# Performance work log

Measured on AMD Instinct MI355X. Metric: run time of the kernel, lower is better.

The kernel has to match this reference:

```python
import jax, jax.numpy as jnp
import numpy as np

B, S, C = 4, 2048, 1024
E, H = 1024, 16
D = E // H  # head_dim = 64


def setup_inputs() -> dict:
    key = jax.random.key(0)
    k1, k2, k3, k4, k5 = jax.random.split(key, 5)
    s = 1.0 / np.sqrt(C)
    return {
        "x": jax.random.normal(k1, (B, S, C), dtype=jnp.float32),
        "w_qkv": jax.random.uniform(k2, (C, 3 * E), minval=-s, maxval=s, dtype=jnp.float32),
        "b_qkv": jax.random.uniform(k3, (3 * E,), minval=-s, maxval=s, dtype=jnp.float32),
        "w_out": jax.random.uniform(k4, (E, E), minval=-1.0 / np.sqrt(E), maxval=1.0 / np.sqrt(E), dtype=jnp.float32),
        "b_out": jax.random.uniform(k5, (E,), minval=-1.0 / np.sqrt(E), maxval=1.0 / np.sqrt(E), dtype=jnp.float32),
    }


def reference(x, w_qkv, b_qkv, w_out, b_out):
    b, s, _ = x.shape
    qkv = x @ w_qkv + b_qkv                      # [B,S,3E]
    qkv = qkv.reshape(b, s, 3, H, D)
    q = qkv[:, :, 0].transpose(0, 2, 1, 3)       # [B,H,S,D]
    k = qkv[:, :, 1].transpose(0, 2, 1, 3)
    v = qkv[:, :, 2].transpose(0, 2, 1, 3)
    scale = jnp.asarray(D, x.dtype) ** 0.5
    scores = jnp.einsum("bhqd,bhkd->bhqk", q, k) / scale
    attn = jax.nn.softmax(scores, axis=-1)       # dropout is identity in eval mode
    out = jnp.einsum("bhqk,bhkd->bhqd", attn, v)
    out = out.transpose(0, 2, 1, 3).reshape(b, s, E)
    return out @ w_out + b_out
```

## Files before the change

kernel.cpp:

```cpp
#include <hip/hip_runtime.h>


typedef _Float16 f16;
typedef f16 f16x2 __attribute__((ext_vector_type(2)));
typedef f16 f16x4 __attribute__((ext_vector_type(4)));
typedef f16 f16x8 __attribute__((ext_vector_type(8)));
typedef float f32x4 __attribute__((ext_vector_type(4)));

typedef const __attribute__((address_space(1))) void* gas_ptr;
typedef __attribute__((address_space(3))) void* lds_ptr;

__device__ __forceinline__ void load_lds16(const void* g, void* s) {
  __builtin_amdgcn_global_load_lds((gas_ptr)g, (lds_ptr)s, 16, 0, 0);
}

__device__ __forceinline__ f32x4 mfma16(f16x8 a, f16x8 b, f32x4 c) {
  return __builtin_amdgcn_mfma_f32_16x16x32_f16(a, b, c, 0, 0, 0);
}

__device__ __forceinline__ f32x4 mfma16k16(f16x4 a, f16x4 b, f32x4 c) {
  return __builtin_amdgcn_mfma_f32_16x16x16f16(a, b, c, 0, 0, 0);
}

__device__ __forceinline__ f16x2 pk2(float a, float b) {
  return __builtin_bit_cast(f16x2, __builtin_amdgcn_cvt_pkrtz(a, b));
}

__global__ __launch_bounds__(256) void cvt_x(const float* __restrict__ in, f16* __restrict__ out) {
  int i = blockIdx.x * 256 + threadIdx.x;
  const float4* p = (const float4*)in;
  float4 a = p[2 * i], b = p[2 * i + 1];
  f16x8 o;
  o[0] = (f16)a.x; o[1] = (f16)a.y; o[2] = (f16)a.z; o[3] = (f16)a.w;
  o[4] = (f16)b.x; o[5] = (f16)b.y; o[6] = (f16)b.z; o[7] = (f16)b.w;
  *(f16x8*)(out + 8 * (long)i) = o;
}

__global__ __launch_bounds__(256) void tconv(const float* __restrict__ in, f16* __restrict__ out,
                                             int R, int C) {
  __shared__ float t[32][33];
  int c0 = blockIdx.x * 32, r0 = blockIdx.y * 32;
  int tx = threadIdx.x, ty = threadIdx.y;
#pragma unroll
  for (int j = 0; j < 4; ++j)
    t[ty + 8 * j][tx] = in[(long)(r0 + ty + 8 * j) * C + c0 + tx];
  __syncthreads();
#pragma unroll
  for (int j = 0; j < 4; ++j)
    out[(long)(c0 + ty + 8 * j) * R + r0 + tx] = (f16)t[tx][ty + 8 * j];
}

__global__ __launch_bounds__(256) void qkv_gemm(const f16* __restrict__ A, const f16* __restrict__ BT,
                                                const float* __restrict__ bias,
                                                f16* __restrict__ Qs, f16* __restrict__ Kk,
                                                f16* __restrict__ Vt) {
  __shared__ __align__(16) f16 lA[128 * 32];
  __shared__ __align__(16) f16 lB[128 * 32];
  const int K = 1024;
  int tid = threadIdx.x, w = tid >> 6, lane = tid & 63, l16 = lane & 15, quad = lane >> 4;
  int wm = (w >> 1) * 64, wn = (w & 1) * 64;
  int blockM = blockIdx.x * 128, blockN = blockIdx.y * 128;
  f32x4 acc[4][4] = {};

  for (int k0 = 0; k0 < K; k0 += 32) {
    __syncthreads();
#pragma unroll
    for (int i = 0; i < 2; ++i) {
      int c = (i * 4 + w) * 64 + lane;
      load_lds16(A + (blockM + (c >> 2)) * K + k0 + (c & 3) * 8, lA + (i * 4 + w) * 512);
      load_lds16(BT + (blockN + (c >> 2)) * K + k0 + (c & 3) * 8, lB + (i * 4 + w) * 512);
    }
    __syncthreads();
    f16x8 af[4], bf[4];
#pragma unroll
    for (int mb = 0; mb < 4; ++mb) af[mb] = *(const f16x8*)&lA[(wm + mb * 16 + l16) * 32 + quad * 8];
#pragma unroll
    for (int nb = 0; nb < 4; ++nb) bf[nb] = *(const f16x8*)&lB[(wn + nb * 16 + l16) * 32 + quad * 8];
#pragma unroll
    for (int mb = 0; mb < 4; ++mb)
#pragma unroll
      for (int nb = 0; nb < 4; ++nb)
        acc[mb][nb] = mfma16(af[mb], bf[nb], acc[mb][nb]);
  }

  int which = blockIdx.y >> 3;
  const float SCALE = 0.18033688011112042f;
#pragma unroll
  for (int nb = 0; nb < 4; ++nb) {
    int col = blockN + wn + nb * 16 + l16;
    int hd = col & 1023, h = hd >> 6, d = hd & 63;
    float bv = bias[col];
#pragma unroll
    for (int mb = 0; mb < 4; ++mb) {
      int row0 = blockM + wm + mb * 16 + quad * 4;
      int b = row0 >> 11, s0 = row0 & 2047;
      if (which == 2) {
        f16x2 a = pk2(acc[mb][nb][0] + bv, acc[mb][nb][1] + bv);
        f16x2 c = pk2(acc[mb][nb][2] + bv, acc[mb][nb][3] + bv);
        *(f16x4*)&Vt[((b * 16 + h) * 64 + d) * 2048 + s0] =
            __builtin_shufflevector(a, c, 0, 1, 2, 3);
      } else if (which == 0) {
#pragma unroll
        for (int r = 0; r < 4; ++r)
          Qs[((b * 16 + h) * 2048 + s0 + r) * 64 + d] = (f16)((acc[mb][nb][r] + bv) * SCALE);
      } else {
#pragma unroll
        for (int r = 0; r < 4; ++r)
          Kk[((b * 16 + h) * 2048 + s0 + r) * 64 + d] = (f16)(acc[mb][nb][r] + bv);
      }
    }
  }
}

__global__ __launch_bounds__(256) void attn(const f16* __restrict__ Qs, const f16* __restrict__ Kk,
                                            const f16* __restrict__ Vt, f16* __restrict__ ctx) {
  __shared__ __align__(16) f16 lK[2][64 * 72];
  __shared__ __align__(16) f16 lV[2][64 * 72];
  int qt = blockIdx.x, bh = blockIdx.y;
  int tid = threadIdx.x, lane = tid & 63, l16 = lane & 15, quad = lane >> 4;
  int w = tid >> 6;
  const f16* Qbase = Qs + ((long)bh * 2048 + qt * 256 + w * 64) * 64;
  const f16* Kbh = Kk + (long)bh * 2048 * 64;
  const f16* Vbh = Vt + (long)bh * 64 * 2048;

  f16x8 qf[4][2];
#pragma unroll
  for (int rb = 0; rb < 4; ++rb)
#pragma unroll
    for (int ks = 0; ks < 2; ++ks)
      qf[rb][ks] = *(const f16x8*)(Qbase + (rb * 16 + l16) * 64 + ks * 32 + quad * 8);

  f32x4 of[4][4] = {};
  f32x4 osum[4] = {};
  const f16 one = (f16)1.f;
  const f16x4 vone = {one, one, one, one};

  int c0 = tid, c1 = 256 + tid;
  int r0s = c0 >> 3, o0 = (c0 & 7) * 8;
  int r1s = c1 >> 3, o1 = (c1 & 7) * 8;

  *(float4*)&lK[0][r0s * 72 + o0] = *(const float4*)(Kbh + r0s * 64 + o0);
  *(float4*)&lK[0][r1s * 72 + o1] = *(const float4*)(Kbh + r1s * 64 + o1);
  *(float4*)&lV[0][r0s * 72 + o0] = *(const float4*)(Vbh + (long)r0s * 2048 + o0);
  *(float4*)&lV[0][r1s * 72 + o1] = *(const float4*)(Vbh + (long)r1s * 2048 + o1);
  __syncthreads();

  for (int kt = 0; kt < 32; ++kt) {
    int cur = kt & 1, nxt = cur ^ 1;

    float4 pk0, pk1, pv0, pv1;
    if (kt < 31) {
      int kb0 = (kt + 1) * 64;
      pk0 = *(const float4*)(Kbh + (kb0 + r0s) * 64 + o0);
      pk1 = *(const float4*)(Kbh + (kb0 + r1s) * 64 + o1);
      pv0 = *(const float4*)(Vbh + (long)r0s * 2048 + kb0 + o0);
      pv1 = *(const float4*)(Vbh + (long)r1s * 2048 + kb0 + o1);
    }

#pragma unroll
    for (int kb = 0; kb < 4; ++kb) {
      f16x8 kf0 = *(const f16x8*)&lK[cur][(kb * 16 + l16) * 72 + quad * 8];
      f16x8 kf1 = *(const f16x8*)&lK[cur][(kb * 16 + l16) * 72 + 32 + quad * 8];

      f16x4 pa[4];
#pragma unroll
      for (int rb = 0; rb < 4; ++rb) {
        f32x4 z = {};
        z = mfma16(kf0, qf[rb][0], z);
        z = mfma16(kf1, qf[rb][1], z);
        float p0 = __builtin_amdgcn_exp2f(z[0]);
        float p1 = __builtin_amdgcn_exp2f(z[1]);
        float p2 = __builtin_amdgcn_exp2f(z[2]);
        float p3 = __builtin_amdgcn_exp2f(z[3]);
        pa[rb] = __builtin_shufflevector(pk2(p0, p1), pk2(p2, p3), 0, 1, 2, 3);
      }

#pragma unroll
      for (int db = 0; db < 4; ++db) {
        f16x4 vf = *(const f16x4*)&lV[cur][(db * 16 + l16) * 72 + kb * 16 + quad * 4];
#pragma unroll
        for (int rb = 0; rb < 4; ++rb)
          of[rb][db] = mfma16k16(pa[rb], vf, of[rb][db]);
      }
#pragma unroll
      for (int rb = 0; rb < 4; ++rb)
        osum[rb] = mfma16k16(pa[rb], vone, osum[rb]);
    }

    if (kt < 31) {
      *(float4*)&lK[nxt][r0s * 72 + o0] = pk0;
      *(float4*)&lK[nxt][r1s * 72 + o1] = pk1;
      *(float4*)&lV[nxt][r0s * 72 + o0] = pv0;
      *(float4*)&lV[nxt][r1s * 72 + o1] = pv1;
      __syncthreads();
    }
  }

  int b = bh >> 4, h = bh & 15;
  long token0 = (long)b * 2048 + qt * 256 + w * 64;
#pragma unroll
  for (int rb = 0; rb < 4; ++rb) {
    float inv[4];
#pragma unroll
    for (int r = 0; r < 4; ++r) inv[r] = 1.0f / osum[rb][r];
#pragma unroll
    for (int db = 0; db < 4; ++db)
#pragma unroll
      for (int r = 0; r < 4; ++r)
        ctx[(token0 + rb * 16 + quad * 4 + r) * 1024 + h * 64 + db * 16 + l16] =
            (f16)(of[rb][db][r] * inv[r]);
  }
}

__global__ __launch_bounds__(256) void proj_gemm(const f16* __restrict__ A, const f16* __restrict__ BT,
                                                 const float* __restrict__ bias,
                                                 float* __restrict__ out) {
  __shared__ __align__(16) f16 lA[128 * 32];
  __shared__ __align__(16) f16 lB[128 * 32];
  const int K = 1024;
  int tid = threadIdx.x, w = tid >> 6, lane = tid & 63, l16 = lane & 15, quad = lane >> 4;
  int wm = (w >> 1) * 64, wn = (w & 1) * 64;
  int blockM = blockIdx.x * 128, blockN = blockIdx.y * 128;
  f32x4 acc[4][4] = {};

  for (int k0 = 0; k0 < K; k0 += 32) {
    __syncthreads();
#pragma unroll
    for (int i = 0; i < 2; ++i) {
      int c = (i * 4 + w) * 64 + lane;
      load_lds16(A + (blockM + (c >> 2)) * K + k0 + (c & 3) * 8, lA + (i * 4 + w) * 512);
      load_lds16(BT + (blockN + (c >> 2)) * K + k0 + (c & 3) * 8, lB + (i * 4 + w) * 512);
    }
    __syncthreads();
    f16x8 af[4], bf[4];
#pragma unroll
    for (int mb = 0; mb < 4; ++mb) af[mb] = *(const f16x8*)&lA[(wm + mb * 16 + l16) * 32 + quad * 8];
#pragma unroll
    for (int nb = 0; nb < 4; ++nb) bf[nb] = *(const f16x8*)&lB[(wn + nb * 16 + l16) * 32 + quad * 8];
#pragma unroll
    for (int mb = 0; mb < 4; ++mb)
#pragma unroll
      for (int nb = 0; nb < 4; ++nb)
        acc[mb][nb] = mfma16(af[mb], bf[nb], acc[mb][nb]);
  }

#pragma unroll
  for (int nb = 0; nb < 4; ++nb) {
    int col = blockN + wn + nb * 16 + l16;
    float bv = bias[col];
#pragma unroll
    for (int mb = 0; mb < 4; ++mb) {
#pragma unroll
      for (int r = 0; r < 4; ++r) {
        int row = blockM + wm + mb * 16 + quad * 4 + r;
        out[(long)row * 1024 + col] = acc[mb][nb][r] + bv;
      }
    }
  }
}

extern "C" void kernel_launch(void* const* d_in, const int* in_sizes, int n_in,
                              void* d_out, int out_size, void* d_ws, size_t ws_size,
                              hipStream_t stream) {
  const float* x     = (const float*)d_in[0];
  const float* w_qkv = (const float*)d_in[1];
  const float* b_qkv = (const float*)d_in[2];
  const float* w_out = (const float*)d_in[3];
  const float* b_out = (const float*)d_in[4];
  float* out = (float*)d_out;

  char* ws = (char*)d_ws;
  f16* xh    = (f16*)(ws);
  f16* ctx   = (f16*)(ws);
  f16* wqkvT = (f16*)(ws + 16777216);
  f16* woutT = (f16*)(ws + 23068672);
  f16* Qs    = (f16*)(ws + 25165824);
  f16* Kk    = (f16*)(ws + 41943040);
  f16* Vt    = (f16*)(ws + 58720256);

  cvt_x<<<4096, 256, 0, stream>>>(x, xh);
  tconv<<<dim3(96, 32), dim3(32, 8), 0, stream>>>(w_qkv, wqkvT, 1024, 3072);
  tconv<<<dim3(32, 32), dim3(32, 8), 0, stream>>>(w_out, woutT, 1024, 1024);
  qkv_gemm<<<dim3(64, 24), 256, 0, stream>>>(xh, wqkvT, b_qkv, Qs, Kk, Vt);
  attn<<<dim3(8, 64), 256, 0, stream>>>(Qs, Kk, Vt, ctx);
  proj_gemm<<<dim3(64, 8), 256, 0, stream>>>(ctx, woutT, b_out, out);
}
```

Before: 296.4 us.

## Swizzle GEMM block order, widen attention to 512 threads with K=32 PV MFMAs

```diff
diff --git a/kernel.cpp b/kernel.cpp
--- a/kernel.cpp
+++ b/kernel.cpp
@@ -16,10 +16,6 @@
 
 __device__ __forceinline__ f32x4 mfma16(f16x8 a, f16x8 b, f32x4 c) {
   return __builtin_amdgcn_mfma_f32_16x16x32_f16(a, b, c, 0, 0, 0);
-}
-
-__device__ __forceinline__ f32x4 mfma16k16(f16x4 a, f16x4 b, f32x4 c) {
-  return __builtin_amdgcn_mfma_f32_16x16x16f16(a, b, c, 0, 0, 0);
 }
 
 __device__ __forceinline__ f16x2 pk2(float a, float b) {
@@ -59,7 +55,11 @@
   const int K = 1024;
   int tid = threadIdx.x, w = tid >> 6, lane = tid & 63, l16 = lane & 15, quad = lane >> 4;
   int wm = (w >> 1) * 64, wn = (w & 1) * 64;
-  int blockM = blockIdx.x * 128, blockN = blockIdx.y * 128;
+  int id = blockIdx.y * gridDim.x + blockIdx.x;
+  int cpx = (gridDim.x * gridDim.y) >> 3;
+  int swz = (id & 7) * cpx + (id >> 3);
+  int bx = swz & 63, by = swz >> 6;
+  int blockM = bx * 128, blockN = by * 128;
   f32x4 acc[4][4] = {};
 
   for (int k0 = 0; k0 < K; k0 += 32) {
@@ -83,7 +83,7 @@
         acc[mb][nb] = mfma16(af[mb], bf[nb], acc[mb][nb]);
   }
 
-  int which = blockIdx.y >> 3;
+  int which = by >> 3;
   const float SCALE = 0.18033688011112042f;
 #pragma unroll
   for (int nb = 0; nb < 4; ++nb) {
@@ -112,94 +112,96 @@
   }
 }
 
-__global__ __launch_bounds__(256) void attn(const f16* __restrict__ Qs, const f16* __restrict__ Kk,
-                                            const f16* __restrict__ Vt, f16* __restrict__ ctx) {
+__global__ __launch_bounds__(512, 4) void attn(const f16* __restrict__ Qs, const f16* __restrict__ Kk,
+                                               const f16* __restrict__ Vt, f16* __restrict__ ctx) {
   __shared__ __align__(16) f16 lK[2][64 * 72];
   __shared__ __align__(16) f16 lV[2][64 * 72];
   int qt = blockIdx.x, bh = blockIdx.y;
   int tid = threadIdx.x, lane = tid & 63, l16 = lane & 15, quad = lane >> 4;
   int w = tid >> 6;
-  const f16* Qbase = Qs + ((long)bh * 2048 + qt * 256 + w * 64) * 64;
+  const f16* Qbase = Qs + ((long)bh * 2048 + qt * 256 + w * 32) * 64;
   const f16* Kbh = Kk + (long)bh * 2048 * 64;
   const f16* Vbh = Vt + (long)bh * 64 * 2048;
 
-  f16x8 qf[4][2];
-#pragma unroll
-  for (int rb = 0; rb < 4; ++rb)
+  f16x8 qf[2][2];
+#pragma unroll
+  for (int rb = 0; rb < 2; ++rb)
 #pragma unroll
     for (int ks = 0; ks < 2; ++ks)
       qf[rb][ks] = *(const f16x8*)(Qbase + (rb * 16 + l16) * 64 + ks * 32 + quad * 8);
 
-  f32x4 of[4][4] = {};
-  f32x4 osum[4] = {};
+  f32x4 of[2][4] = {};
+  f32x4 osum[2] = {};
   const f16 one = (f16)1.f;
-  const f16x4 vone = {one, one, one, one};
-
-  int c0 = tid, c1 = 256 + tid;
-  int r0s = c0 >> 3, o0 = (c0 & 7) * 8;
-  int r1s = c1 >> 3, o1 = (c1 & 7) * 8;
-
-  *(float4*)&lK[0][r0s * 72 + o0] = *(const float4*)(Kbh + r0s * 64 + o0);
-  *(float4*)&lK[0][r1s * 72 + o1] = *(const float4*)(Kbh + r1s * 64 + o1);
-  *(float4*)&lV[0][r0s * 72 + o0] = *(const float4*)(Vbh + (long)r0s * 2048 + o0);
-  *(float4*)&lV[0][r1s * 72 + o1] = *(const float4*)(Vbh + (long)r1s * 2048 + o1);
+  const f16x8 vone8 = {one, one, one, one, one, one, one, one};
+
+  int rs = tid >> 3, o = (tid & 7) * 8;
+
+  *(float4*)&lK[0][rs * 72 + o] = *(const float4*)(Kbh + rs * 64 + o);
+  *(float4*)&lV[0][rs * 72 + o] = *(const float4*)(Vbh + (long)rs * 2048 + o);
   __syncthreads();
 
   for (int kt = 0; kt < 32; ++kt) {
     int cur = kt & 1, nxt = cur ^ 1;
 
-    float4 pk0, pk1, pv0, pv1;
+    float4 pk0, pv0;
     if (kt < 31) {
       int kb0 = (kt + 1) * 64;
-      pk0 = *(const float4*)(Kbh + (kb0 + r0s) * 64 + o0);
-      pk1 = *(const float4*)(Kbh + (kb0 + r1s) * 64 + o1);
-      pv0 = *(const float4*)(Vbh + (long)r0s * 2048 + kb0 + o0);
-      pv1 = *(const float4*)(Vbh + (long)r1s * 2048 + kb0 + o1);
-    }
-
-#pragma unroll
-    for (int kb = 0; kb < 4; ++kb) {
-      f16x8 kf0 = *(const f16x8*)&lK[cur][(kb * 16 + l16) * 72 + quad * 8];
-      f16x8 kf1 = *(const f16x8*)&lK[cur][(kb * 16 + l16) * 72 + 32 + quad * 8];
-
-      f16x4 pa[4];
-#pragma unroll
-      for (int rb = 0; rb < 4; ++rb) {
-        f32x4 z = {};
-        z = mfma16(kf0, qf[rb][0], z);
-        z = mfma16(kf1, qf[rb][1], z);
-        float p0 = __builtin_amdgcn_exp2f(z[0]);
-        float p1 = __builtin_amdgcn_exp2f(z[1]);
-        float p2 = __builtin_amdgcn_exp2f(z[2]);
-        float p3 = __builtin_amdgcn_exp2f(z[3]);
-        pa[rb] = __builtin_shufflevector(pk2(p0, p1), pk2(p2, p3), 0, 1, 2, 3);
-      }
+      pk0 = *(const float4*)(Kbh + (kb0 + rs) * 64 + o);
+      pv0 = *(const float4*)(Vbh + (long)rs * 2048 + kb0 + o);
+    }
+
+    __builtin_amdgcn_s_setprio(1);
+#pragma unroll
+    for (int kp = 0; kp < 2; ++kp) {
+      f16x4 pah[2][2];
+#pragma unroll
+      for (int kbh = 0; kbh < 2; ++kbh) {
+        int kb = kp * 2 + kbh;
+        f16x8 kf0 = *(const f16x8*)&lK[cur][(kb * 16 + l16) * 72 + quad * 8];
+        f16x8 kf1 = *(const f16x8*)&lK[cur][(kb * 16 + l16) * 72 + 32 + quad * 8];
+#pragma unroll
+        for (int rb = 0; rb < 2; ++rb) {
+          f32x4 z = {};
+          z = mfma16(kf0, qf[rb][0], z);
+          z = mfma16(kf1, qf[rb][1], z);
+          float p0 = __builtin_amdgcn_exp2f(z[0]);
+          float p1 = __builtin_amdgcn_exp2f(z[1]);
+          float p2 = __builtin_amdgcn_exp2f(z[2]);
+          float p3 = __builtin_amdgcn_exp2f(z[3]);
+          pah[rb][kbh] = __builtin_shufflevector(pk2(p0, p1), pk2(p2, p3), 0, 1, 2, 3);
+        }
+      }
+      f16x8 pa[2];
+      pa[0] = __builtin_shufflevector(pah[0][0], pah[0][1], 0, 1, 2, 3, 4, 5, 6, 7);
+      pa[1] = __builtin_shufflevector(pah[1][0], pah[1][1], 0, 1, 2, 3, 4, 5, 6, 7);
 
 #pragma unroll
       for (int db = 0; db < 4; ++db) {
-        f16x4 vf = *(const f16x4*)&lV[cur][(db * 16 + l16) * 72 + kb * 16 + quad * 4];
-#pragma unroll
-        for (int rb = 0; rb < 4; ++rb)
-          of[rb][db] = mfma16k16(pa[rb], vf, of[rb][db]);
-      }
-#pragma unroll
-      for (int rb = 0; rb < 4; ++rb)
-        osum[rb] = mfma16k16(pa[rb], vone, osum[rb]);
-    }
+        f16x4 va = *(const f16x4*)&lV[cur][(db * 16 + l16) * 72 + kp * 32 + quad * 4];
+        f16x4 vb = *(const f16x4*)&lV[cur][(db * 16 + l16) * 72 + kp * 32 + 16 + quad * 4];
+        f16x8 vf = __builtin_shufflevector(va, vb, 0, 1, 2, 3, 4, 5, 6, 7);
+#pragma unroll
+        for (int rb = 0; rb < 2; ++rb)
+          of[rb][db] = mfma16(pa[rb], vf, of[rb][db]);
+      }
+#pragma unroll
+      for (int rb = 0; rb < 2; ++rb)
+        osum[rb] = mfma16(pa[rb], vone8, osum[rb]);
+    }
+    __builtin_amdgcn_s_setprio(0);
 
     if (kt < 31) {
-      *(float4*)&lK[nxt][r0s * 72 + o0] = pk0;
-      *(float4*)&lK[nxt][r1s * 72 + o1] = pk1;
-      *(float4*)&lV[nxt][r0s * 72 + o0] = pv0;
-      *(float4*)&lV[nxt][r1s * 72 + o1] = pv1;
+      *(float4*)&lK[nxt][rs * 72 + o] = pk0;
+      *(float4*)&lV[nxt][rs * 72 + o] = pv0;
       __syncthreads();
     }
   }
 
   int b = bh >> 4, h = bh & 15;
-  long token0 = (long)b * 2048 + qt * 256 + w * 64;
-#pragma unroll
-  for (int rb = 0; rb < 4; ++rb) {
+  long token0 = (long)b * 2048 + qt * 256 + w * 32;
+#pragma unroll
+  for (int rb = 0; rb < 2; ++rb) {
     float inv[4];
 #pragma unroll
     for (int r = 0; r < 4; ++r) inv[r] = 1.0f / osum[rb][r];
@@ -220,7 +222,11 @@
   const int K = 1024;
   int tid = threadIdx.x, w = tid >> 6, lane = tid & 63, l16 = lane & 15, quad = lane >> 4;
   int wm = (w >> 1) * 64, wn = (w & 1) * 64;
-  int blockM = blockIdx.x * 128, blockN = blockIdx.y * 128;
+  int id = blockIdx.y * gridDim.x + blockIdx.x;
+  int cpx = (gridDim.x * gridDim.y) >> 3;
+  int swz = (id & 7) * cpx + (id >> 3);
+  int bx = swz & 63, by = swz >> 6;
+  int blockM = bx * 128, blockN = by * 128;
   f32x4 acc[4][4] = {};
 
   for (int k0 = 0; k0 < K; k0 += 32) {
@@ -282,6 +288,6 @@
   tconv<<<dim3(96, 32), dim3(32, 8), 0, stream>>>(w_qkv, wqkvT, 1024, 3072);
   tconv<<<dim3(32, 32), dim3(32, 8), 0, stream>>>(w_out, woutT, 1024, 1024);
   qkv_gemm<<<dim3(64, 24), 256, 0, stream>>>(xh, wqkvT, b_qkv, Qs, Kk, Vt);
-  attn<<<dim3(8, 64), 256, 0, stream>>>(Qs, Kk, Vt, ctx);
+  attn<<<dim3(8, 64), 512, 0, stream>>>(Qs, Kk, Vt, ctx);
   proj_gemm<<<dim3(64, 8), 256, 0, stream>>>(ctx, woutT, b_out, out);
 }
```

New measurement: 278.9 us. -5.9%, faster.
